# Kernel optimization log

Hardware: AMD Instinct MI355X
Metric: run time of the kernel (lower is better)

Reference implementation:

```python
import jax, jax.numpy as jnp
import numpy as np

H = 4096      # hidden_dim
D = 128       # head_dim
NQ = 32       # n_q_heads = H // D
NKV = 8       # n_kv_heads (GQA)
EPS = 1e-5
ROTARY_BASE = 10000.0


def _rope(x):
    # Non-interleaved (GPT-NeoX / flash-attn) rotary over full head_dim.
    # x: [B, S, nheads, D]
    S = x.shape[1]
    half = D // 2
    inv_freq = 1.0 / (ROTARY_BASE ** (jnp.arange(0, D, 2, dtype=jnp.float32) / D))  # [D/2]
    freqs = jnp.arange(S, dtype=jnp.float32)[:, None] * inv_freq[None, :]           # [S, D/2]
    cos = jnp.cos(freqs)[None, :, None, :].astype(x.dtype)
    sin = jnp.sin(freqs)[None, :, None, :].astype(x.dtype)
    x1, x2 = x[..., :half], x[..., half:]
    return jnp.concatenate([x1 * cos - x2 * sin, x2 * cos + x1 * sin], axis=-1)


def setup_inputs() -> dict:
    key = jax.random.key(0)
    ks = jax.random.split(key, 7)
    B, S = 1, 2048
    std = 0.02
    return {
        "hidden_states": jax.random.normal(ks[0], (B, S, H), dtype=jnp.float32),
        "ln_w": jnp.ones((H,), dtype=jnp.float32),
        "ln_b": jnp.zeros((H,), dtype=jnp.float32),
        "wq": jax.random.normal(ks[1], (H, NQ * D), dtype=jnp.float32) * std,
        "wk": jax.random.normal(ks[2], (H, NKV * D), dtype=jnp.float32) * std,
        "wv": jax.random.normal(ks[3], (H, NKV * D), dtype=jnp.float32) * std,
        "wo": jax.random.normal(ks[4], (NQ * D, H), dtype=jnp.float32) * std,
    }


def reference(hidden_states, ln_w, ln_b, wq, wk, wv, wo):
    B, S, _ = hidden_states.shape
    # LayerNorm
    mu = jnp.mean(hidden_states, axis=-1, keepdims=True)
    var = jnp.mean(jnp.square(hidden_states - mu), axis=-1, keepdims=True)
    x = (hidden_states - mu) * jax.lax.rsqrt(var + EPS) * ln_w + ln_b
    # Fused QKV projection
    q = (x @ wq).reshape(B, S, NQ, D)
    k = (x @ wk).reshape(B, S, NKV, D)
    v = (x @ wv).reshape(B, S, NKV, D)
    # Rotary embedding on q and k
    q = _rope(q)
    k = _rope(k)
    # GQA: repeat kv heads
    rep = NQ // NKV
    k_r = jnp.repeat(k, rep, axis=2)  # [B, S, NQ, D]
    v_r = jnp.repeat(v, rep, axis=2)
    # Causal attention, softmax_scale = 1/sqrt(D)
    scale = 1.0 / np.sqrt(D)
    scores = jnp.einsum("bshd,bthd->bhst", q, k_r) * scale  # [B, NQ, S, S]
    causal = jnp.tril(jnp.ones((S, S), dtype=bool))
    scores = jnp.where(causal[None, None], scores, jnp.finfo(scores.dtype).min)
    p = jax.nn.softmax(scores, axis=-1)
    attn = jnp.einsum("bhst,bthd->bshd", p, v_r)  # [B, S, NQ, D]
    # Output projection (dropout p=0 in eval)
    out = attn.reshape(B, S, NQ * D) @ wo
    return out
```

## Files before the change

kernel.cpp:

```cpp
#include <hip/hip_runtime.h>
#include <hip/hip_bf16.h>

#define HDIM 4096
#define DHEAD 128
#define NQH 32
#define NKVH 8
#define SEQ 2048
#define QKVN 6144

typedef __bf16 bf16x8 __attribute__((ext_vector_type(8)));
typedef unsigned short ushort8 __attribute__((ext_vector_type(8)));
typedef float f32x4 __attribute__((ext_vector_type(4)));
typedef float f32x16 __attribute__((ext_vector_type(16)));
typedef unsigned int u32x4 __attribute__((ext_vector_type(4)));

#define WAIT_VM(N) __builtin_amdgcn_s_waitcnt(0xF70 | (N))

__device__ inline unsigned short f2bf(float f) {
    unsigned u = __float_as_uint(f);
    u += 0x7fffu + ((u >> 16) & 1u);
    return (unsigned short)(u >> 16);
}

__device__ inline float bf2f(unsigned short u) {
    return __uint_as_float(((unsigned)u) << 16);
}

__device__ inline unsigned cvtpk(float lo, float hi) {
    unsigned r;
    asm("v_cvt_pk_bf16_f32 %0, %1, %2" : "=v"(r) : "v"(lo), "v"(hi));
    return r;
}

__device__ inline void gload16(const void* g, void* l) {
    __builtin_amdgcn_global_load_lds(
        (const __attribute__((address_space(1))) unsigned int*)g,
        (__attribute__((address_space(3))) unsigned int*)l, 16, 0, 0);
}

__global__ void transpose_convert(const float* __restrict__ in, unsigned short* __restrict__ out,
                                  int K, int N) {
    __shared__ float tile[64][33];
    const int n0 = blockIdx.x * 32, k0 = blockIdx.y * 64;
    const int tx = threadIdx.x, ty = threadIdx.y;
    #pragma unroll
    for (int r = 0; r < 8; r++)
        tile[ty + r * 8][tx] = in[(size_t)(k0 + ty + r * 8) * N + n0 + tx];
    __syncthreads();
    #pragma unroll
    for (int r = 0; r < 4; r++) {
        int n = ty + r * 8;
        unsigned v = (unsigned)f2bf(tile[tx * 2][n]) |
                     ((unsigned)f2bf(tile[tx * 2 + 1][n]) << 16);
        *(unsigned*)&out[(size_t)(n0 + n) * K + k0 + tx * 2] = v;
    }
}

__global__ void transpose_v(const unsigned short* __restrict__ qkvb,
                            unsigned short* __restrict__ vbt) {
    __shared__ unsigned short tile[32][34];
    const int s0 = blockIdx.x * 32, d0 = blockIdx.y * 32, hv = blockIdx.z;
    const int tx = threadIdx.x, ty = threadIdx.y;
    for (int r = 0; r < 32; r += 8)
        tile[ty + r][tx] = qkvb[(size_t)(s0 + ty + r) * QKVN + 5120 + hv * DHEAD + d0 + tx];
    __syncthreads();
    for (int r = 0; r < 32; r += 8)
        vbt[((size_t)hv * DHEAD + d0 + ty + r) * SEQ + s0 + tx] = tile[tx][ty + r];
}

__global__ __launch_bounds__(256) void layernorm_kernel(
    const float* __restrict__ hs, const float* __restrict__ w, const float* __restrict__ b,
    unsigned short* __restrict__ xb) {
    const int s = blockIdx.x;
    const float* row = hs + (size_t)s * HDIM;
    const int t = threadIdx.x;
    float vals[16];
    float sum = 0.f, sq = 0.f;
    for (int j = 0; j < 16; j++) {
        float v = row[j * 256 + t];
        vals[j] = v; sum += v; sq += v * v;
    }
    for (int off = 1; off < 64; off <<= 1) {
        sum += __shfl_xor(sum, off);
        sq  += __shfl_xor(sq, off);
    }
    __shared__ float ps[4], pq[4];
    if ((t & 63) == 0) { ps[t >> 6] = sum; pq[t >> 6] = sq; }
    __syncthreads();
    sum = ps[0] + ps[1] + ps[2] + ps[3];
    sq  = pq[0] + pq[1] + pq[2] + pq[3];
    const float mu = sum * (1.0f / HDIM);
    const float var = sq * (1.0f / HDIM) - mu * mu;
    const float rs = rsqrtf(var + 1e-5f);
    for (int j = 0; j < 16; j++) {
        int i = j * 256 + t;
        xb[(size_t)s * HDIM + i] = f2bf((vals[j] - mu) * rs * w[i] + b[i]);
    }
}

__global__ __launch_bounds__(512, 2) void gemm8p(
    const unsigned short* __restrict__ A, const unsigned short* __restrict__ Bt,
    void* __restrict__ Cout, int N, int lda, int Keff, int nbx, int cBf16) {
    __shared__ __align__(16) unsigned short Abuf[2 * 2 * 256 * 32];
    __shared__ __align__(16) unsigned short Bbuf[2 * 2 * 256 * 32];

    const int inner = blockIdx.x;
    const int cbx = nbx >> 3;
    const int xcd = inner & 7, k = inner >> 3;
    const int bx = xcd * cbx + (k % cbx);
    const int by = k / cbx;
    const int row0 = by * 256, col0 = bx * 256;

    const int t = threadIdx.x, lane = t & 63, w = t >> 6;
    const int wr = w >> 2, wc = w & 3;
    const int r16 = lane & 15, kq = lane >> 4;

    const int srow = t >> 2;
    const int scsw = (t & 3) ^ ((srow >> 1) & 3);
    const unsigned short* aStage = A  + (size_t)(row0 + srow) * lda + scsw * 8;
    const unsigned short* bStage = Bt + (size_t)(col0 + srow) * lda + scsw * 8;
    const size_t half = 128 * (size_t)lda;
    const int wdst = w * 512;

    const int NT = Keff / 64;

#define STAGE(p0, ldsbuf, bufidx, kh, kt) do {                                  \
        const unsigned short* _g = (p0) + (size_t)(kt) * 64 + (kh) * 32;        \
        gload16(_g,        &ldsbuf[((bufidx) * 2 + (kh)) * 8192 + wdst]);       \
        gload16(_g + half, &ldsbuf[((bufidx) * 2 + (kh)) * 8192 + 4096 + wdst]);\
    } while (0)

#define LDA4(dst, bufidx, kh, ih) {                                             \
        _Pragma("unroll") for (int i = 0; i < 4; i++) {                         \
            int arow = wr * 128 + (ih) * 64 + i * 16 + r16;                     \
            dst[i] = *(const bf16x8*)&Abuf[((bufidx) * 2 + (kh)) * 8192 +       \
                     arow * 32 + (kq ^ ((arow >> 1) & 3)) * 8];                 \
        } }

#define LDB4(dst, bufidx, kh) {                                                 \
        _Pragma("unroll") for (int j = 0; j < 4; j++) {                         \
            int brow = wc * 64 + j * 16 + r16;                                  \
            dst[j] = *(const bf16x8*)&Bbuf[((bufidx) * 2 + (kh)) * 8192 +       \
                     brow * 32 + (kq ^ ((brow >> 1) & 3)) * 8];                 \
        } }

#define MM16(ih, av, bv) {                                                      \
        __builtin_amdgcn_s_setprio(1);                                          \
        _Pragma("unroll") for (int i = 0; i < 4; i++)                           \
            _Pragma("unroll") for (int j = 0; j < 4; j++)                       \
                acc[(ih) * 4 + i][j] = __builtin_amdgcn_mfma_f32_16x16x32_bf16( \
                    av[i], bv[j], acc[(ih) * 4 + i][j], 0, 0, 0);               \
        __builtin_amdgcn_s_setprio(0); }

    STAGE(aStage, Abuf, 0, 0, 0);
    STAGE(bStage, Bbuf, 0, 0, 0);
    STAGE(aStage, Abuf, 0, 1, 0);
    STAGE(bStage, Bbuf, 0, 1, 0);
    WAIT_VM(4);
    __builtin_amdgcn_s_barrier();

    f32x4 acc[8][4] = {};
    for (int kt = 0; kt < NT; ++kt) {
        const int cur = kt & 1, nxt = cur ^ 1;
        const bool nl = (kt + 1 < NT);
        bf16x8 a0[4], a1[4], bv[4];
        LDA4(a0, cur, 0, 0);
        LDB4(bv, cur, 0);
        if (nl) STAGE(aStage, Abuf, nxt, 0, kt + 1);
        MM16(0, a0, bv);
        LDA4(a1, cur, 0, 1);
        if (nl) STAGE(bStage, Bbuf, nxt, 0, kt + 1);
        MM16(1, a1, bv);
        if (nl) WAIT_VM(4); else WAIT_VM(0);
        __builtin_amdgcn_s_barrier();
        LDA4(a0, cur, 1, 0);
        LDB4(bv, cur, 1);
        if (nl) STAGE(aStage, Abuf, nxt, 1, kt + 1);
        MM16(0, a0, bv);
        LDA4(a1, cur, 1, 1);
        if (nl) STAGE(bStage, Bbuf, nxt, 1, kt + 1);
        MM16(1, a1, bv);
        if (nl) {
            WAIT_VM(4);
            __builtin_amdgcn_s_barrier();
        }
    }

    if (cBf16) {
        unsigned short* C = (unsigned short*)Cout;
        #pragma unroll
        for (int i = 0; i < 8; i++)
            #pragma unroll
            for (int j = 0; j < 4; j++)
                #pragma unroll
                for (int r = 0; r < 4; r++) {
                    int row = row0 + wr * 128 + i * 16 + kq * 4 + r;
                    int col = col0 + wc * 64 + j * 16 + r16;
                    C[(size_t)row * N + col] = f2bf(acc[i][j][r]);
                }
    } else {
        float* C = (float*)Cout;
        #pragma unroll
        for (int i = 0; i < 8; i++)
            #pragma unroll
            for (int j = 0; j < 4; j++)
                #pragma unroll
                for (int r = 0; r < 4; r++) {
                    int row = row0 + wr * 128 + i * 16 + kq * 4 + r;
                    int col = col0 + wc * 64 + j * 16 + r16;
                    C[(size_t)row * N + col] = acc[i][j][r];
                }
    }
#undef STAGE
#undef LDA4
#undef LDB4
#undef MM16
}

__global__ __launch_bounds__(512, 2) void gemm8n(
    const unsigned short* __restrict__ A, const unsigned short* __restrict__ Bt,
    float* __restrict__ C, int N, int lda, int Keff, int nbx) {
    __shared__ __align__(16) unsigned short Abuf[3][256 * 64];
    __shared__ __align__(16) unsigned short Bbuf[3][128 * 64];

    const int inner = blockIdx.x;
    const int cbx = nbx >> 3;
    const int xcd = inner & 7, kk = inner >> 3;
    const int bx = xcd * cbx + (kk % cbx);
    const int by = kk / cbx;
    const int row0 = by * 256, col0 = bx * 128;

    const int t = threadIdx.x, lane = t & 63, w = t >> 6;
    const int wr = w >> 1, wc = w & 1;
    const int r16 = lane & 15, kq = lane >> 4;

    const int srow = t >> 3;
    const int scsw = (t & 7) ^ (srow & 7);
    const unsigned short* aStage = A  + (size_t)(row0 + srow) * lda + scsw * 8;
    const unsigned short* bStage = Bt + (size_t)(col0 + srow) * lda + scsw * 8;
    const size_t rstep = 64 * (size_t)lda;

    const int NT = Keff / 64;

#define NSTG_H0(bufi, kt) {                                                     \
        gload16(aStage + (size_t)(kt) * 64,             &Abuf[bufi][0 * 4096 + w * 512]); \
        gload16(aStage + (size_t)(kt) * 64 + rstep,     &Abuf[bufi][1 * 4096 + w * 512]); \
        gload16(bStage + (size_t)(kt) * 64,             &Bbuf[bufi][0 * 4096 + w * 512]); }
#define NSTG_H1(bufi, kt) {                                                     \
        gload16(aStage + (size_t)(kt) * 64 + 2 * rstep, &Abuf[bufi][2 * 4096 + w * 512]); \
        gload16(aStage + (size_t)(kt) * 64 + 3 * rstep, &Abuf[bufi][3 * 4096 + w * 512]); \
        gload16(bStage + (size_t)(kt) * 64 + rstep,     &Bbuf[bufi][1 * 4096 + w * 512]); }

#define NLDA(dst, bufi, kh) { _Pragma("unroll") for (int i = 0; i < 4; i++) {   \
        int ar = wr * 64 + i * 16 + r16;                                        \
        dst[i] = *(const bf16x8*)&Abuf[bufi][ar * 64 + (((kh) * 4 + kq) ^ (ar & 7)) * 8]; } }
#define NLDB(dst, bufi, kh) { _Pragma("unroll") for (int j = 0; j < 4; j++) {   \
        int br = wc * 64 + j * 16 + r16;                                        \
        dst[j] = *(const bf16x8*)&Bbuf[bufi][br * 64 + (((kh) * 4 + kq) ^ (br & 7)) * 8]; } }

#define MMN(av, bv) {                                                           \
        __builtin_amdgcn_s_setprio(1);                                          \
        _Pragma("unroll") for (int i = 0; i < 4; i++)                           \
            _Pragma("unroll") for (int j = 0; j < 4; j++)                       \
                acc[i][j] = __builtin_amdgcn_mfma_f32_16x16x32_bf16(            \
                    av[i], bv[j], acc[i][j], 0, 0, 0);                          \
        __builtin_amdgcn_s_setprio(0); }

    NSTG_H0(0, 0); NSTG_H1(0, 0);
    NSTG_H0(1, 1); NSTG_H1(1, 1);
    WAIT_VM(6);
    __builtin_amdgcn_s_barrier();

    f32x4 acc[4][4] = {};
    for (int kt = 0; kt < NT; ++kt) {
        const int cur = kt % 3, nx2 = (kt + 2) % 3;
        const bool pf = (kt + 2) < NT;
        bf16x8 av[4], bv[4];
        NLDA(av, cur, 0);
        NLDB(bv, cur, 0);
        if (pf) NSTG_H0(nx2, kt + 2);
        MMN(av, bv);
        NLDA(av, cur, 1);
        NLDB(bv, cur, 1);
        if (pf) NSTG_H1(nx2, kt + 2);
        MMN(av, bv);
        if (kt + 1 < NT) {
            if (pf) WAIT_VM(6); else WAIT_VM(0);
            __builtin_amdgcn_s_barrier();
        }
    }

    #pragma unroll
    for (int i = 0; i < 4; i++)
        #pragma unroll
        for (int j = 0; j < 4; j++)
            #pragma unroll
            for (int r = 0; r < 4; r++) {
                int row = row0 + wr * 64 + i * 16 + kq * 4 + r;
                int col = col0 + wc * 64 + j * 16 + r16;
                C[(size_t)row * N + col] = acc[i][j][r];
            }
#undef NSTG_H0
#undef NSTG_H1
#undef NLDA
#undef NLDB
#undef MMN
}

__global__ void rope_convert(const unsigned short* __restrict__ qkvb,
                             unsigned short* __restrict__ qb, unsigned short* __restrict__ kb) {
    const int s = blockIdx.x;
    const int head = blockIdx.y;
    const int d = threadIdx.x;
    const float SCALE = 0.08838834764831845f;
    const float NLOG = -0.14391156831212787f;
    float f = (float)s * __expf((float)d * NLOG);
    float sn, c;
    __sincosf(f, &sn, &c);
    if (head < NQH) {
        const unsigned short* src = qkvb + (size_t)s * QKVN + head * DHEAD;
        float x1 = bf2f(src[d]), x2 = bf2f(src[d + 64]);
        unsigned short* dst = qb + ((size_t)head * SEQ + s) * DHEAD;
        dst[d]      = f2bf((x1 * c - x2 * sn) * SCALE);
        dst[d + 64] = f2bf((x2 * c + x1 * sn) * SCALE);
    } else {
        const int hk = head - NQH;
        const unsigned short* src = qkvb + (size_t)s * QKVN + 4096 + hk * DHEAD;
        float x1 = bf2f(src[d]), x2 = bf2f(src[d + 64]);
        unsigned short* dst = kb + ((size_t)hk * SEQ + s) * DHEAD;
        dst[d]      = f2bf(x1 * c - x2 * sn);
        dst[d + 64] = f2bf(x2 * c + x1 * sn);
    }
}

__global__ __launch_bounds__(256, 2) void attention_kernel(
    const unsigned short* __restrict__ Q, const unsigned short* __restrict__ K,
    const unsigned short* __restrict__ Vt, unsigned short* __restrict__ O) {
    __shared__ __align__(16) unsigned short Ks[64 * 128];
    __shared__ __align__(16) unsigned short Vs[128 * 64];
    const int h = blockIdx.x & 31;
    const int p = 15 - (blockIdx.x >> 5);
    const int t = threadIdx.x, lane = t & 63, w = t >> 6;
    const int q31 = lane & 31, h2 = lane >> 5;
    const int q0w = p * 128 + w * 32;
    const int kbw = 2 * p + (w >> 1);
    const int kbmax = 2 * p + 1;
    const int hkv = h >> 2;

    bf16x8 qf[8];
    {
        const unsigned short* qrow = Q + ((size_t)h * SEQ + q0w + q31) * DHEAD + h2 * 8;
        #pragma unroll
        for (int ds = 0; ds < 8; ds++) qf[ds] = *(const bf16x8*)&qrow[ds * 16];
    }

    f32x16 oacc[4] = {};
    float m_r = -1e30f, l_r = 0.f;

    const unsigned short* Kg = K + (size_t)hkv * SEQ * DHEAD;
    const unsigned short* Vg = Vt + (size_t)hkv * DHEAD * SEQ;

    const int krow = t >> 4, kch = t & 15;
    const int vrow = t >> 3, vch = t & 7;
    ushort8 kreg[4], vreg[4];
    #pragma unroll
    for (int pp = 0; pp < 4; pp++) {
        kreg[pp] = *(const ushort8*)&Kg[(size_t)(pp * 16 + krow) * DHEAD + kch * 8];
        vreg[pp] = *(const ushort8*)&Vg[(size_t)(pp * 32 + vrow) * SEQ + vch * 8];
    }

    for (int kb = 0; kb <= kbmax; ++kb) {
        __syncthreads();
        #pragma unroll
        for (int pp = 0; pp < 4; pp++) {
            int row = pp * 16 + krow;
            *(ushort8*)&Ks[row * 128 + ((kch ^ (row & 7)) * 8)] = kreg[pp];
            int vr = pp * 32 + vrow;
            *(ushort8*)&Vs[vr * 64 + ((vch ^ (vr & 7)) * 8)] = vreg[pp];
        }
        if (kb < kbmax) {
            #pragma unroll
            for (int pp = 0; pp < 4; pp++) {
                kreg[pp] = *(const ushort8*)&Kg[(size_t)((kb + 1) * 64 + pp * 16 + krow) * DHEAD + kch * 8];
                vreg[pp] = *(const ushort8*)&Vg[(size_t)(pp * 32 + vrow) * SEQ + (kb + 1) * 64 + vch * 8];
            }
        }
        __syncthreads();
        if (kb > kbw) continue;

        f32x16 s0 = {}, s1 = {};
        #pragma unroll
        for (int ds = 0; ds < 8; ds++) {
            int r0 = q31;
            int c0 = (ds * 2 + h2) ^ (r0 & 7);
            bf16x8 kf0 = *(const bf16x8*)&Ks[r0 * 128 + c0 * 8];
            s0 = __builtin_amdgcn_mfma_f32_32x32x16_bf16(kf0, qf[ds], s0, 0, 0, 0);
            int r1 = 32 + q31;
            int c1 = (ds * 2 + h2) ^ (r1 & 7);
            bf16x8 kf1 = *(const bf16x8*)&Ks[r1 * 128 + c1 * 8];
            s1 = __builtin_amdgcn_mfma_f32_32x32x16_bf16(kf1, qf[ds], s1, 0, 0, 0);
        }
        if (kb == kbw) {
            const int qg = q0w + q31;
            #pragma unroll
            for (int r = 0; r < 16; r++) {
                int kpos = (r & 3) + 8 * (r >> 2) + 4 * h2;
                s0[r] = (kb * 64 + kpos > qg) ? -1e30f : s0[r];
                s1[r] = (kb * 64 + 32 + kpos > qg) ? -1e30f : s1[r];
            }
        }
        float pm = -1e30f;
        #pragma unroll
        for (int r = 0; r < 16; r++) pm = fmaxf(pm, fmaxf(s0[r], s1[r]));
        pm = fmaxf(pm, __shfl_xor(pm, 32));
        bool grow = pm > m_r + 8.f;
        if (__any(grow)) {
            float mn = fmaxf(m_r, pm);
            float sc = __expf(m_r - mn);
            l_r *= sc;
            float scr[16];
            #pragma unroll
            for (int r = 0; r < 16; r++) scr[r] = __shfl(sc, (r & 3) + 8 * (r >> 2) + 4 * h2);
            #pragma unroll
            for (int nt = 0; nt < 4; nt++)
                #pragma unroll
                for (int r = 0; r < 16; r++) oacc[nt][r] *= scr[r];
            m_r = mn;
        }
        float sum = 0.f;
        #pragma unroll
        for (int r = 0; r < 16; r++) {
            s0[r] = __expf(s0[r] - m_r); sum += s0[r];
            s1[r] = __expf(s1[r] - m_r); sum += s1[r];
        }
        sum += __shfl_xor(sum, 32);
        l_r += sum;
        unsigned ow0[8], ow1[8];
        #pragma unroll
        for (int a = 0; a < 4; a++) {
            ow0[a * 2 + 0] = cvtpk(s0[4 * a + 0], s0[4 * a + 1]);
            ow0[a * 2 + 1] = cvtpk(s0[4 * a + 2], s0[4 * a + 3]);
            ow1[a * 2 + 0] = cvtpk(s1[4 * a + 0], s1[4 * a + 1]);
            ow1[a * 2 + 1] = cvtpk(s1[4 * a + 2], s1[4 * a + 3]);
        }
        unsigned pw0[8], pw1[8];
        #pragma unroll
        for (int i = 0; i < 8; i++) {
            pw0[i] = __shfl_xor((int)ow0[i], 32);
            pw1[i] = __shfl_xor((int)ow1[i], 32);
        }
        bf16x8 pf[4];
        const bool lo = (h2 == 0);
        #pragma unroll
        for (int sub = 0; sub < 2; sub++) {
            int b0 = 2 * sub, b1 = 2 * sub + 1;
            u32x4 t0, t1;
            t0.x = lo ? ow0[b0 * 2 + 0] : pw0[b1 * 2 + 0];
            t0.y = lo ? ow0[b0 * 2 + 1] : pw0[b1 * 2 + 1];
            t0.z = lo ? pw0[b0 * 2 + 0] : ow0[b1 * 2 + 0];
            t0.w = lo ? pw0[b0 * 2 + 1] : ow0[b1 * 2 + 1];
            pf[sub] = __builtin_bit_cast(bf16x8, t0);
            t1.x = lo ? ow1[b0 * 2 + 0] : pw1[b1 * 2 + 0];
            t1.y = lo ? ow1[b0 * 2 + 1] : pw1[b1 * 2 + 1];
            t1.z = lo ? pw1[b0 * 2 + 0] : ow1[b1 * 2 + 0];
            t1.w = lo ? pw1[b0 * 2 + 1] : ow1[b1 * 2 + 1];
            pf[2 + sub] = __builtin_bit_cast(bf16x8, t1);
        }
        #pragma unroll
        for (int nt = 0; nt < 4; nt++) {
            int vr2 = nt * 32 + q31;
            #pragma unroll
            for (int kt16 = 0; kt16 < 4; kt16++) {
                int vc2 = (kt16 * 2 + h2) ^ (vr2 & 7);
                bf16x8 vf = *(const bf16x8*)&Vs[vr2 * 64 + vc2 * 8];
                oacc[nt] = __builtin_amdgcn_mfma_f32_32x32x16_bf16(pf[kt16], vf, oacc[nt], 0, 0, 0);
            }
        }
    }
    float inv = 1.0f / l_r;
    float invr[16];
    #pragma unroll
    for (int r = 0; r < 16; r++) invr[r] = __shfl(inv, (r & 3) + 8 * (r >> 2) + 4 * h2);
    #pragma unroll
    for (int nt = 0; nt < 4; nt++)
        #pragma unroll
        for (int r = 0; r < 16; r++) {
            int qg = q0w + (r & 3) + 8 * (r >> 2) + 4 * h2;
            O[(size_t)qg * HDIM + h * DHEAD + nt * 32 + q31] = f2bf(oacc[nt][r] * invr[r]);
        }
}

extern "C" void kernel_launch(void* const* d_in, const int* in_sizes, int n_in,
                              void* d_out, int out_size, void* d_ws, size_t ws_size,
                              hipStream_t stream) {
    const float* hs  = (const float*)d_in[0];
    const float* lnw = (const float*)d_in[1];
    const float* lnb = (const float*)d_in[2];
    const float* wq  = (const float*)d_in[3];
    const float* wk  = (const float*)d_in[4];
    const float* wv  = (const float*)d_in[5];
    const float* wo  = (const float*)d_in[6];
    float* out = (float*)d_out;

    char* ws = (char*)d_ws;
    size_t off = 0;
    auto alloc = [&](size_t bytes) {
        void* p = ws + off;
        off += (bytes + 255) & ~(size_t)255;
        return p;
    };
    unsigned short* xb   = (unsigned short*)alloc((size_t)SEQ * HDIM * 2);
    unsigned short* wqT  = (unsigned short*)alloc((size_t)HDIM * (NQH * DHEAD) * 2);
    unsigned short* wkT  = (unsigned short*)alloc((size_t)HDIM * (NKVH * DHEAD) * 2);
    unsigned short* wvT  = (unsigned short*)alloc((size_t)HDIM * (NKVH * DHEAD) * 2);
    unsigned short* woT  = (unsigned short*)alloc((size_t)(NQH * DHEAD) * HDIM * 2);
    unsigned short* qkvb = (unsigned short*)alloc((size_t)SEQ * QKVN * 2);
    unsigned short* qbuf = (unsigned short*)alloc((size_t)NQH * SEQ * DHEAD * 2);
    unsigned short* kbuf = (unsigned short*)alloc((size_t)NKVH * SEQ * DHEAD * 2);
    unsigned short* vbt  = (unsigned short*)alloc((size_t)NKVH * DHEAD * SEQ * 2);
    unsigned short* attnb = qkvb;

    dim3 tb(32, 8);
    transpose_convert<<<dim3(4096 / 32, 4096 / 64), tb, 0, stream>>>(wq, wqT, 4096, 4096);
    transpose_convert<<<dim3(1024 / 32, 4096 / 64), tb, 0, stream>>>(wk, wkT, 4096, 1024);
    transpose_convert<<<dim3(1024 / 32, 4096 / 64), tb, 0, stream>>>(wv, wvT, 4096, 1024);
    transpose_convert<<<dim3(4096 / 32, 4096 / 64), tb, 0, stream>>>(wo, woT, 4096, 4096);

    layernorm_kernel<<<SEQ, 256, 0, stream>>>(hs, lnw, lnb, xb);

    gemm8p<<<(2048 / 256) * (QKVN / 256), 512, 0, stream>>>(
        xb, wqT, qkvb, QKVN, 4096, 4096, QKVN / 256, 1);

    rope_convert<<<dim3(SEQ, NQH + NKVH), 64, 0, stream>>>(qkvb, qbuf, kbuf);
    transpose_v<<<dim3(SEQ / 32, DHEAD / 32, NKVH), tb, 0, stream>>>(qkvb, vbt);

    attention_kernel<<<NQH * 16, 256, 0, stream>>>(qbuf, kbuf, vbt, attnb);

    gemm8n<<<(2048 / 256) * (4096 / 128), 512, 0, stream>>>(
        attnb, woT, out, 4096, 4096, 4096, 4096 / 128);
}
```

Baseline: 320.9 us.

## Restructure both GEMMs into 4-slot K=32 pipelines with prefetch depth three

Both the QKV GEMM and the output-projection GEMM now use a 4-slot ring of K=32 LDS tiles with loads issued three tiles ahead. This replaces the old double-buffered K=64 split-half scheme and the 3-buffer K=64 scheme. The aim is to hide global-load latency better and to give the two GEMMs a uniform staging layout. The trade-off is twice as many barriers per K step (one per 32 instead of about two per 64) and different vmcnt bookkeeping at the loop tail. LDS footprint stays about the same.

```diff
diff --git a/kernel.cpp b/kernel.cpp
--- a/kernel.cpp
+++ b/kernel.cpp
@@ -98,11 +98,11 @@
     }
 }
 
-__global__ __launch_bounds__(512, 2) void gemm8p(
+__global__ __launch_bounds__(512, 2) void gemm10(
     const unsigned short* __restrict__ A, const unsigned short* __restrict__ Bt,
     void* __restrict__ Cout, int N, int lda, int Keff, int nbx, int cBf16) {
-    __shared__ __align__(16) unsigned short Abuf[2 * 2 * 256 * 32];
-    __shared__ __align__(16) unsigned short Bbuf[2 * 2 * 256 * 32];
+    __shared__ __align__(16) unsigned short Abuf[4 * 256 * 32];
+    __shared__ __align__(16) unsigned short Bbuf[4 * 256 * 32];
 
     const int inner = blockIdx.x;
     const int cbx = nbx >> 3;
@@ -117,71 +117,56 @@
 
     const int srow = t >> 2;
     const int scsw = (t & 3) ^ ((srow >> 1) & 3);
-    const unsigned short* aStage = A  + (size_t)(row0 + srow) * lda + scsw * 8;
-    const unsigned short* bStage = Bt + (size_t)(col0 + srow) * lda + scsw * 8;
-    const size_t half = 128 * (size_t)lda;
+    const unsigned short* aS = A  + (size_t)(row0 + srow) * lda + scsw * 8;
+    const unsigned short* bS = Bt + (size_t)(col0 + srow) * lda + scsw * 8;
+    const size_t h128 = 128 * (size_t)lda;
     const int wdst = w * 512;
 
-    const int NT = Keff / 64;
-
-#define STAGE(p0, ldsbuf, bufidx, kh, kt) do {                                  \
-        const unsigned short* _g = (p0) + (size_t)(kt) * 64 + (kh) * 32;        \
-        gload16(_g,        &ldsbuf[((bufidx) * 2 + (kh)) * 8192 + wdst]);       \
-        gload16(_g + half, &ldsbuf[((bufidx) * 2 + (kh)) * 8192 + 4096 + wdst]);\
-    } while (0)
-
-#define LDA4(dst, bufidx, kh, ih) {                                             \
-        _Pragma("unroll") for (int i = 0; i < 4; i++) {                         \
-            int arow = wr * 128 + (ih) * 64 + i * 16 + r16;                     \
-            dst[i] = *(const bf16x8*)&Abuf[((bufidx) * 2 + (kh)) * 8192 +       \
-                     arow * 32 + (kq ^ ((arow >> 1) & 3)) * 8];                 \
-        } }
-
-#define LDB4(dst, bufidx, kh) {                                                 \
-        _Pragma("unroll") for (int j = 0; j < 4; j++) {                         \
-            int brow = wc * 64 + j * 16 + r16;                                  \
-            dst[j] = *(const bf16x8*)&Bbuf[((bufidx) * 2 + (kh)) * 8192 +       \
-                     brow * 32 + (kq ^ ((brow >> 1) & 3)) * 8];                 \
-        } }
-
-#define MM16(ih, av, bv) {                                                      \
-        __builtin_amdgcn_s_setprio(1);                                          \
-        _Pragma("unroll") for (int i = 0; i < 4; i++)                           \
-            _Pragma("unroll") for (int j = 0; j < 4; j++)                       \
-                acc[(ih) * 4 + i][j] = __builtin_amdgcn_mfma_f32_16x16x32_bf16( \
-                    av[i], bv[j], acc[(ih) * 4 + i][j], 0, 0, 0);               \
+    const int NT = Keff / 32;
+
+#define SA10(slot, kt) { const unsigned short* _g = aS + (size_t)(kt) * 32;      \
+        gload16(_g,        &Abuf[(slot) * 8192 + wdst]);                         \
+        gload16(_g + h128, &Abuf[(slot) * 8192 + 4096 + wdst]); }
+#define SB10(slot, kt) { const unsigned short* _g = bS + (size_t)(kt) * 32;      \
+        gload16(_g,        &Bbuf[(slot) * 8192 + wdst]);                         \
+        gload16(_g + h128, &Bbuf[(slot) * 8192 + 4096 + wdst]); }
+#define RA10(dst, slot, ih) { _Pragma("unroll") for (int i = 0; i < 4; i++) {    \
+        int ar = wr * 128 + (ih) * 64 + i * 16 + r16;                            \
+        dst[i] = *(const bf16x8*)&Abuf[(slot) * 8192 + ar * 32 +                 \
+                 (kq ^ ((ar >> 1) & 3)) * 8]; } }
+#define RB10(dst, slot) { _Pragma("unroll") for (int j = 0; j < 4; j++) {        \
+        int br = wc * 64 + j * 16 + r16;                                         \
+        dst[j] = *(const bf16x8*)&Bbuf[(slot) * 8192 + br * 32 +                 \
+                 (kq ^ ((br >> 1) & 3)) * 8]; } }
+#define MM10(ih, av, bv) { __builtin_amdgcn_s_setprio(1);                        \
+        _Pragma("unroll") for (int i = 0; i < 4; i++)                            \
+            _Pragma("unroll") for (int j = 0; j < 4; j++)                        \
+                acc[(ih) * 4 + i][j] = __builtin_amdgcn_mfma_f32_16x16x32_bf16(  \
+                    av[i], bv[j], acc[(ih) * 4 + i][j], 0, 0, 0);                \
         __builtin_amdgcn_s_setprio(0); }
 
-    STAGE(aStage, Abuf, 0, 0, 0);
-    STAGE(bStage, Bbuf, 0, 0, 0);
-    STAGE(aStage, Abuf, 0, 1, 0);
-    STAGE(bStage, Bbuf, 0, 1, 0);
-    WAIT_VM(4);
+    SA10(0, 0); SB10(0, 0);
+    SA10(1, 1); SB10(1, 1);
+    SA10(2, 2); SB10(2, 2);
+    WAIT_VM(8);
     __builtin_amdgcn_s_barrier();
 
     f32x4 acc[8][4] = {};
     for (int kt = 0; kt < NT; ++kt) {
-        const int cur = kt & 1, nxt = cur ^ 1;
-        const bool nl = (kt + 1 < NT);
+        const int cur = kt & 3, st = (kt + 3) & 3;
+        const bool pf = (kt + 3) < NT;
         bf16x8 a0[4], a1[4], bv[4];
-        LDA4(a0, cur, 0, 0);
-        LDB4(bv, cur, 0);
-        if (nl) STAGE(aStage, Abuf, nxt, 0, kt + 1);
-        MM16(0, a0, bv);
-        LDA4(a1, cur, 0, 1);
-        if (nl) STAGE(bStage, Bbuf, nxt, 0, kt + 1);
-        MM16(1, a1, bv);
-        if (nl) WAIT_VM(4); else WAIT_VM(0);
-        __builtin_amdgcn_s_barrier();
-        LDA4(a0, cur, 1, 0);
-        LDB4(bv, cur, 1);
-        if (nl) STAGE(aStage, Abuf, nxt, 1, kt + 1);
-        MM16(0, a0, bv);
-        LDA4(a1, cur, 1, 1);
-        if (nl) STAGE(bStage, Bbuf, nxt, 1, kt + 1);
-        MM16(1, a1, bv);
-        if (nl) {
-            WAIT_VM(4);
+        RA10(a0, cur, 0);
+        RB10(bv, cur);
+        if (pf) SA10(st, kt + 3);
+        MM10(0, a0, bv);
+        RA10(a1, cur, 1);
+        if (pf) SB10(st, kt + 3);
+        MM10(1, a1, bv);
+        if (kt + 1 < NT) {
+            if (kt + 3 < NT) WAIT_VM(8);
+            else if (kt + 3 == NT) WAIT_VM(4);
+            else WAIT_VM(0);
             __builtin_amdgcn_s_barrier();
         }
     }
@@ -211,17 +196,18 @@
                     C[(size_t)row * N + col] = acc[i][j][r];
                 }
     }
-#undef STAGE
-#undef LDA4
-#undef LDB4
-#undef MM16
-}
-
-__global__ __launch_bounds__(512, 2) void gemm8n(
+#undef SA10
+#undef SB10
+#undef RA10
+#undef RB10
+#undef MM10
+}
+
+__global__ __launch_bounds__(512, 2) void gemm10n(
     const unsigned short* __restrict__ A, const unsigned short* __restrict__ Bt,
     float* __restrict__ C, int N, int lda, int Keff, int nbx) {
-    __shared__ __align__(16) unsigned short Abuf[3][256 * 64];
-    __shared__ __align__(16) unsigned short Bbuf[3][128 * 64];
+    __shared__ __align__(16) unsigned short Abuf[4 * 256 * 32];
+    __shared__ __align__(16) unsigned short Bbuf[4 * 128 * 32];
 
     const int inner = blockIdx.x;
     const int cbx = nbx >> 3;
@@ -234,58 +220,54 @@
     const int wr = w >> 1, wc = w & 1;
     const int r16 = lane & 15, kq = lane >> 4;
 
-    const int srow = t >> 3;
-    const int scsw = (t & 7) ^ (srow & 7);
-    const unsigned short* aStage = A  + (size_t)(row0 + srow) * lda + scsw * 8;
-    const unsigned short* bStage = Bt + (size_t)(col0 + srow) * lda + scsw * 8;
-    const size_t rstep = 64 * (size_t)lda;
-
-    const int NT = Keff / 64;
-
-#define NSTG_H0(bufi, kt) {                                                     \
-        gload16(aStage + (size_t)(kt) * 64,             &Abuf[bufi][0 * 4096 + w * 512]); \
-        gload16(aStage + (size_t)(kt) * 64 + rstep,     &Abuf[bufi][1 * 4096 + w * 512]); \
-        gload16(bStage + (size_t)(kt) * 64,             &Bbuf[bufi][0 * 4096 + w * 512]); }
-#define NSTG_H1(bufi, kt) {                                                     \
-        gload16(aStage + (size_t)(kt) * 64 + 2 * rstep, &Abuf[bufi][2 * 4096 + w * 512]); \
-        gload16(aStage + (size_t)(kt) * 64 + 3 * rstep, &Abuf[bufi][3 * 4096 + w * 512]); \
-        gload16(bStage + (size_t)(kt) * 64 + rstep,     &Bbuf[bufi][1 * 4096 + w * 512]); }
-
-#define NLDA(dst, bufi, kh) { _Pragma("unroll") for (int i = 0; i < 4; i++) {   \
-        int ar = wr * 64 + i * 16 + r16;                                        \
-        dst[i] = *(const bf16x8*)&Abuf[bufi][ar * 64 + (((kh) * 4 + kq) ^ (ar & 7)) * 8]; } }
-#define NLDB(dst, bufi, kh) { _Pragma("unroll") for (int j = 0; j < 4; j++) {   \
-        int br = wc * 64 + j * 16 + r16;                                        \
-        dst[j] = *(const bf16x8*)&Bbuf[bufi][br * 64 + (((kh) * 4 + kq) ^ (br & 7)) * 8]; } }
-
-#define MMN(av, bv) {                                                           \
-        __builtin_amdgcn_s_setprio(1);                                          \
-        _Pragma("unroll") for (int i = 0; i < 4; i++)                           \
-            _Pragma("unroll") for (int j = 0; j < 4; j++)                       \
-                acc[i][j] = __builtin_amdgcn_mfma_f32_16x16x32_bf16(            \
-                    av[i], bv[j], acc[i][j], 0, 0, 0);                          \
+    const int srow = t >> 2;
+    const int scsw = (t & 3) ^ ((srow >> 1) & 3);
+    const unsigned short* aS = A  + (size_t)(row0 + srow) * lda + scsw * 8;
+    const unsigned short* bS = Bt + (size_t)(col0 + srow) * lda + scsw * 8;
+    const size_t h128 = 128 * (size_t)lda;
+    const int wdst = w * 512;
+
+    const int NT = Keff / 32;
+
+#define SAN(slot, kt) { const unsigned short* _g = aS + (size_t)(kt) * 32;       \
+        gload16(_g,        &Abuf[(slot) * 8192 + wdst]);                         \
+        gload16(_g + h128, &Abuf[(slot) * 8192 + 4096 + wdst]); }
+#define SBN(slot, kt) { gload16(bS + (size_t)(kt) * 32, &Bbuf[(slot) * 4096 + wdst]); }
+#define RAN(dst, slot) { _Pragma("unroll") for (int i = 0; i < 4; i++) {         \
+        int ar = wr * 64 + i * 16 + r16;                                         \
+        dst[i] = *(const bf16x8*)&Abuf[(slot) * 8192 + ar * 32 +                 \
+                 (kq ^ ((ar >> 1) & 3)) * 8]; } }
+#define RBN(dst, slot) { _Pragma("unroll") for (int j = 0; j < 4; j++) {         \
+        int br = wc * 64 + j * 16 + r16;                                         \
+        dst[j] = *(const bf16x8*)&Bbuf[(slot) * 4096 + br * 32 +                 \
+                 (kq ^ ((br >> 1) & 3)) * 8]; } }
+#define MMN(av, bv) { __builtin_amdgcn_s_setprio(1);                             \
+        _Pragma("unroll") for (int i = 0; i < 4; i++)                            \
+            _Pragma("unroll") for (int j = 0; j < 4; j++)                        \
+                acc[i][j] = __builtin_amdgcn_mfma_f32_16x16x32_bf16(             \
+                    av[i], bv[j], acc[i][j], 0, 0, 0);                           \
         __builtin_amdgcn_s_setprio(0); }
 
-    NSTG_H0(0, 0); NSTG_H1(0, 0);
-    NSTG_H0(1, 1); NSTG_H1(1, 1);
+    SAN(0, 0); SBN(0, 0);
+    SAN(1, 1); SBN(1, 1);
+    SAN(2, 2); SBN(2, 2);
     WAIT_VM(6);
     __builtin_amdgcn_s_barrier();
 
     f32x4 acc[4][4] = {};
     for (int kt = 0; kt < NT; ++kt) {
-        const int cur = kt % 3, nx2 = (kt + 2) % 3;
-        const bool pf = (kt + 2) < NT;
+        const int cur = kt & 3, st = (kt + 3) & 3;
+        const bool pf = (kt + 3) < NT;
         bf16x8 av[4], bv[4];
-        NLDA(av, cur, 0);
-        NLDB(bv, cur, 0);
-        if (pf) NSTG_H0(nx2, kt + 2);
-        MMN(av, bv);
-        NLDA(av, cur, 1);
-        NLDB(bv, cur, 1);
-        if (pf) NSTG_H1(nx2, kt + 2);
+        RAN(av, cur);
+        if (pf) SAN(st, kt + 3);
+        RBN(bv, cur);
+        if (pf) SBN(st, kt + 3);
         MMN(av, bv);
         if (kt + 1 < NT) {
-            if (pf) WAIT_VM(6); else WAIT_VM(0);
+            if (kt + 3 < NT) WAIT_VM(6);
+            else if (kt + 3 == NT) WAIT_VM(3);
+            else WAIT_VM(0);
             __builtin_amdgcn_s_barrier();
         }
     }
@@ -300,10 +282,10 @@
                 int col = col0 + wc * 64 + j * 16 + r16;
                 C[(size_t)row * N + col] = acc[i][j][r];
             }
-#undef NSTG_H0
-#undef NSTG_H1
-#undef NLDA
-#undef NLDB
+#undef SAN
+#undef SBN
+#undef RAN
+#undef RBN
 #undef MMN
 }
 
@@ -528,7 +510,7 @@
 
     layernorm_kernel<<<SEQ, 256, 0, stream>>>(hs, lnw, lnb, xb);
 
-    gemm8p<<<(2048 / 256) * (QKVN / 256), 512, 0, stream>>>(
+    gemm10<<<(2048 / 256) * (QKVN / 256), 512, 0, stream>>>(
         xb, wqT, qkvb, QKVN, 4096, 4096, QKVN / 256, 1);
 
     rope_convert<<<dim3(SEQ, NQH + NKVH), 64, 0, stream>>>(qkvb, qbuf, kbuf);
@@ -536,6 +518,6 @@
 
     attention_kernel<<<NQH * 16, 256, 0, stream>>>(qbuf, kbuf, vbt, attnb);
 
-    gemm8n<<<(2048 / 256) * (4096 / 128), 512, 0, stream>>>(
+    gemm10n<<<(2048 / 256) * (4096 / 128), 512, 0, stream>>>(
         attnb, woT, out, 4096, 4096, 4096, 4096 / 128);
 }
```

Measured after the change: 333.9 us. +4.1%, slower.

## Retile QKV GEMM to 256x192 tiles with reworked B staging

Applied to the files above, without the earlier changes.

The QKV projection GEMM moves from 256x256 tiles to 256x192 tiles. That gives 256 blocks over the 6144 output columns instead of 192, which should fill the CUs more evenly. B is now staged as full 64-wide K rows with an 8-way XOR swizzle, and each wave does 8x3 MFMAs per half-step. Launch bounds drop to one block per CU, and the A/B prefetch schedule is reorganised around this. The trade-off is less reuse per tile and possibly lower occupancy.

```diff
diff --git a/kernel.cpp b/kernel.cpp
--- a/kernel.cpp
+++ b/kernel.cpp
@@ -98,90 +98,82 @@
     }
 }
 
-__global__ __launch_bounds__(512, 2) void gemm8p(
+__global__ __launch_bounds__(512, 1) void gemm11(
     const unsigned short* __restrict__ A, const unsigned short* __restrict__ Bt,
     void* __restrict__ Cout, int N, int lda, int Keff, int nbx, int cBf16) {
     __shared__ __align__(16) unsigned short Abuf[2 * 2 * 256 * 32];
-    __shared__ __align__(16) unsigned short Bbuf[2 * 2 * 256 * 32];
+    __shared__ __align__(16) unsigned short Bbuf[2 * 192 * 64];
 
     const int inner = blockIdx.x;
     const int cbx = nbx >> 3;
     const int xcd = inner & 7, k = inner >> 3;
     const int bx = xcd * cbx + (k % cbx);
     const int by = k / cbx;
-    const int row0 = by * 256, col0 = bx * 256;
+    const int row0 = by * 256, col0 = bx * 192;
 
     const int t = threadIdx.x, lane = t & 63, w = t >> 6;
     const int wr = w >> 2, wc = w & 3;
     const int r16 = lane & 15, kq = lane >> 4;
 
-    const int srow = t >> 2;
-    const int scsw = (t & 3) ^ ((srow >> 1) & 3);
-    const unsigned short* aStage = A  + (size_t)(row0 + srow) * lda + scsw * 8;
-    const unsigned short* bStage = Bt + (size_t)(col0 + srow) * lda + scsw * 8;
-    const size_t half = 128 * (size_t)lda;
+    const int srowA = t >> 2;
+    const int scswA = (t & 3) ^ ((srowA >> 1) & 3);
+    const unsigned short* aS = A + (size_t)(row0 + srowA) * lda + scswA * 8;
+    const int srowB = t >> 3;
+    const int scswB = (t & 7) ^ (srowB & 7);
+    const unsigned short* bS = Bt + (size_t)(col0 + srowB) * lda + scswB * 8;
+    const size_t a128 = 128 * (size_t)lda;
+    const size_t b64 = 64 * (size_t)lda;
     const int wdst = w * 512;
 
     const int NT = Keff / 64;
 
-#define STAGE(p0, ldsbuf, bufidx, kh, kt) do {                                  \
-        const unsigned short* _g = (p0) + (size_t)(kt) * 64 + (kh) * 32;        \
-        gload16(_g,        &ldsbuf[((bufidx) * 2 + (kh)) * 8192 + wdst]);       \
-        gload16(_g + half, &ldsbuf[((bufidx) * 2 + (kh)) * 8192 + 4096 + wdst]);\
-    } while (0)
-
-#define LDA4(dst, bufidx, kh, ih) {                                             \
-        _Pragma("unroll") for (int i = 0; i < 4; i++) {                         \
-            int arow = wr * 128 + (ih) * 64 + i * 16 + r16;                     \
-            dst[i] = *(const bf16x8*)&Abuf[((bufidx) * 2 + (kh)) * 8192 +       \
-                     arow * 32 + (kq ^ ((arow >> 1) & 3)) * 8];                 \
-        } }
-
-#define LDB4(dst, bufidx, kh) {                                                 \
-        _Pragma("unroll") for (int j = 0; j < 4; j++) {                         \
-            int brow = wc * 64 + j * 16 + r16;                                  \
-            dst[j] = *(const bf16x8*)&Bbuf[((bufidx) * 2 + (kh)) * 8192 +       \
-                     brow * 32 + (kq ^ ((brow >> 1) & 3)) * 8];                 \
-        } }
-
-#define MM16(ih, av, bv) {                                                      \
-        __builtin_amdgcn_s_setprio(1);                                          \
-        _Pragma("unroll") for (int i = 0; i < 4; i++)                           \
-            _Pragma("unroll") for (int j = 0; j < 4; j++)                       \
-                acc[(ih) * 4 + i][j] = __builtin_amdgcn_mfma_f32_16x16x32_bf16( \
-                    av[i], bv[j], acc[(ih) * 4 + i][j], 0, 0, 0);               \
+#define SA11(bufi, kh, kt) {                                                        \
+        const unsigned short* _g = aS + (size_t)(kt) * 64 + (kh) * 32;              \
+        gload16(_g,        &Abuf[(bufi) * 16384 + (kh) * 8192 + wdst]);             \
+        gload16(_g + a128, &Abuf[(bufi) * 16384 + (kh) * 8192 + 4096 + wdst]); }
+#define SB11(bufi, kt) {                                                            \
+        const unsigned short* _g = bS + (size_t)(kt) * 64;                          \
+        gload16(_g,            &Bbuf[(bufi) * 12288 + wdst]);                       \
+        gload16(_g + b64,      &Bbuf[(bufi) * 12288 + 4096 + wdst]);                \
+        gload16(_g + 2 * b64,  &Bbuf[(bufi) * 12288 + 8192 + wdst]); }
+#define RA11(dst, bufi, kh) { _Pragma("unroll") for (int i = 0; i < 8; i++) {       \
+        int ar = wr * 128 + i * 16 + r16;                                           \
+        dst[i] = *(const bf16x8*)&Abuf[(bufi) * 16384 + (kh) * 8192 + ar * 32 +     \
+                 (kq ^ ((ar >> 1) & 3)) * 8]; } }
+#define RB11(dst, bufi, kh) { _Pragma("unroll") for (int j = 0; j < 3; j++) {       \
+        int br = wc * 48 + j * 16 + r16;                                            \
+        dst[j] = *(const bf16x8*)&Bbuf[(bufi) * 12288 + br * 64 +                   \
+                 ((((kh) * 4) + kq) ^ (br & 7)) * 8]; } }
+#define MM11(av, bv) { __builtin_amdgcn_s_setprio(1);                               \
+        _Pragma("unroll") for (int i = 0; i < 8; i++)                               \
+            _Pragma("unroll") for (int j = 0; j < 3; j++)                           \
+                acc[i][j] = __builtin_amdgcn_mfma_f32_16x16x32_bf16(                \
+                    av[i], bv[j], acc[i][j], 0, 0, 0);                              \
         __builtin_amdgcn_s_setprio(0); }
 
-    STAGE(aStage, Abuf, 0, 0, 0);
-    STAGE(bStage, Bbuf, 0, 0, 0);
-    STAGE(aStage, Abuf, 0, 1, 0);
-    STAGE(bStage, Bbuf, 0, 1, 0);
-    WAIT_VM(4);
+    SA11(0, 0, 0);
+    SB11(0, 0);
+    SA11(0, 1, 0);
+    WAIT_VM(2);
     __builtin_amdgcn_s_barrier();
 
-    f32x4 acc[8][4] = {};
+    f32x4 acc[8][3] = {};
     for (int kt = 0; kt < NT; ++kt) {
         const int cur = kt & 1, nxt = cur ^ 1;
-        const bool nl = (kt + 1 < NT);
-        bf16x8 a0[4], a1[4], bv[4];
-        LDA4(a0, cur, 0, 0);
-        LDB4(bv, cur, 0);
-        if (nl) STAGE(aStage, Abuf, nxt, 0, kt + 1);
-        MM16(0, a0, bv);
-        LDA4(a1, cur, 0, 1);
-        if (nl) STAGE(bStage, Bbuf, nxt, 0, kt + 1);
-        MM16(1, a1, bv);
-        if (nl) WAIT_VM(4); else WAIT_VM(0);
+        const bool pf = (kt + 1 < NT);
+        bf16x8 av[8], bv[3];
+        RA11(av, cur, 0);
+        RB11(bv, cur, 0);
+        if (pf) SA11(nxt, 0, kt + 1);
+        MM11(av, bv);
+        if (pf) WAIT_VM(2); else WAIT_VM(0);
         __builtin_amdgcn_s_barrier();
-        LDA4(a0, cur, 1, 0);
-        LDB4(bv, cur, 1);
-        if (nl) STAGE(aStage, Abuf, nxt, 1, kt + 1);
-        MM16(0, a0, bv);
-        LDA4(a1, cur, 1, 1);
-        if (nl) STAGE(bStage, Bbuf, nxt, 1, kt + 1);
-        MM16(1, a1, bv);
-        if (nl) {
-            WAIT_VM(4);
+        RA11(av, cur, 1);
+        RB11(bv, cur, 1);
+        if (pf) { SB11(nxt, kt + 1); SA11(nxt, 1, kt + 1); }
+        MM11(av, bv);
+        if (pf) {
+            WAIT_VM(2);
             __builtin_amdgcn_s_barrier();
         }
     }
@@ -191,11 +183,11 @@
         #pragma unroll
         for (int i = 0; i < 8; i++)
             #pragma unroll
-            for (int j = 0; j < 4; j++)
+            for (int j = 0; j < 3; j++)
                 #pragma unroll
                 for (int r = 0; r < 4; r++) {
                     int row = row0 + wr * 128 + i * 16 + kq * 4 + r;
-                    int col = col0 + wc * 64 + j * 16 + r16;
+                    int col = col0 + wc * 48 + j * 16 + r16;
                     C[(size_t)row * N + col] = f2bf(acc[i][j][r]);
                 }
     } else {
@@ -203,18 +195,19 @@
         #pragma unroll
         for (int i = 0; i < 8; i++)
             #pragma unroll
-            for (int j = 0; j < 4; j++)
+            for (int j = 0; j < 3; j++)
                 #pragma unroll
                 for (int r = 0; r < 4; r++) {
                     int row = row0 + wr * 128 + i * 16 + kq * 4 + r;
-                    int col = col0 + wc * 64 + j * 16 + r16;
+                    int col = col0 + wc * 48 + j * 16 + r16;
                     C[(size_t)row * N + col] = acc[i][j][r];
                 }
     }
-#undef STAGE
-#undef LDA4
-#undef LDB4
-#undef MM16
+#undef SA11
+#undef SB11
+#undef RA11
+#undef RB11
+#undef MM11
 }
 
 __global__ __launch_bounds__(512, 2) void gemm8n(
@@ -528,8 +521,8 @@
 
     layernorm_kernel<<<SEQ, 256, 0, stream>>>(hs, lnw, lnb, xb);
 
-    gemm8p<<<(2048 / 256) * (QKVN / 256), 512, 0, stream>>>(
-        xb, wqT, qkvb, QKVN, 4096, 4096, QKVN / 256, 1);
+    gemm11<<<(2048 / 256) * (QKVN / 192), 512, 0, stream>>>(
+        xb, wqT, qkvb, QKVN, 4096, 4096, QKVN / 192, 1);
 
     rope_convert<<<dim3(SEQ, NQH + NKVH), 64, 0, stream>>>(qkvb, qbuf, kbuf);
     transpose_v<<<dim3(SEQ / 32, DHEAD / 32, NKVH), tb, 0, stream>>>(qkvb, vbt);
```

Result: faster. 313.3 us (-2.3%).
